# Performance work log

Measured on AMD Instinct MI355X. Metric: run time of the kernel, lower is better.

The kernel has to match this reference:

```python
import jax, jax.numpy as jnp
import numpy as np

EPS = 1e-5
D, C, T, H = 512, 256, 2, 2  # d_model, d_ctx, tokens, heads
HD = D // H                   # head dim


def _ln(x, g, b):
    m = x.mean(-1, keepdims=True)
    v = ((x - m) ** 2).mean(-1, keepdims=True)
    return (x - m) / jnp.sqrt(v + EPS) * g + b


def setup_inputs() -> dict:
    key = jax.random.key(0)
    ks = jax.random.split(key, 16)
    B, L = 8, 4096
    w = lambda k, s: (jax.random.normal(k, s, jnp.float32) * 0.02)
    Hc, H2 = 512, 1024  # ctx-head hidden = max(D,C); mix hidden = 2*D
    return {
        "x": jax.random.normal(ks[0], (B, L, D), jnp.float32),
        "context": jax.random.normal(ks[1], (B, C), jnp.float32),
        "pad_valid_mask": jax.random.bernoulli(ks[2], 0.9, (B, L)),
        "film_ln_g": jnp.ones(D), "film_ln_b": jnp.zeros(D),
        "film_w": w(ks[3], (2 * D, C)), "film_b": jnp.zeros(2 * D),
        "concat_w": w(ks[4], (D, D + C)), "concat_b": jnp.zeros(D),
        "concat_ln_g": jnp.ones(D), "concat_ln_b": jnp.zeros(D),
        "ctx_w1": w(ks[5], (Hc, C)), "ctx_b1": jnp.zeros(Hc),
        "ctx_w2": w(ks[6], (T * D, Hc)), "ctx_b2": jnp.zeros(T * D),
        "q_ln_g": jnp.ones(D), "q_ln_b": jnp.zeros(D),
        "in_proj_w": w(ks[7], (3 * D, D)), "in_proj_b": jnp.zeros(3 * D),
        "out_proj_w": w(ks[8], (D, D)), "out_proj_b": jnp.zeros(D),
        "mix_w1": w(ks[9], (H2, 4 * D)), "mix_b1": jnp.zeros(H2),
        "mix_w2": w(ks[10], (D, H2)), "mix_b2": jnp.zeros(D),
        "out_ln_g": jnp.ones(D), "out_ln_b": jnp.zeros(D),
        "gate_w": w(ks[11], (D, C)), "gate_b": jnp.zeros(D),
    }


def reference(x, context, pad_valid_mask,
              film_ln_g, film_ln_b, film_w, film_b,
              concat_w, concat_b, concat_ln_g, concat_ln_b,
              ctx_w1, ctx_b1, ctx_w2, ctx_b2,
              q_ln_g, q_ln_b, in_proj_w, in_proj_b, out_proj_w, out_proj_b,
              mix_w1, mix_b1, mix_w2, mix_b2,
              out_ln_g, out_ln_b, gate_w, gate_b):
    B, L, _ = x.shape
    film_gain, alpha_max = 1.0, 1.0
    # 1) HyperFiLM: base = (1 + gain*gamma) * LN(x) + gain*beta
    gb = context @ film_w.T + film_b                      # [B, 2D]
    gamma, beta = gb[:, :D], gb[:, D:]
    base = (1.0 + film_gain * gamma)[:, None, :] * _ln(x, film_ln_g, film_ln_b) \
           + (film_gain * beta)[:, None, :]
    # 2) Concat path
    ctx_exp = jnp.broadcast_to(context[:, None, :], (B, L, C))
    z = jnp.concatenate([x, ctx_exp], axis=-1)            # [B, L, D+C]
    upd_c = _ln(jax.nn.relu(z @ concat_w.T + concat_b), concat_ln_g, concat_ln_b)
    # 3) Cross-attn path: context -> T tokens
    h = jax.nn.gelu(context @ ctx_w1.T + ctx_b1, approximate=False)
    ctx_tok = (h @ ctx_w2.T + ctx_b2).reshape(B, T, D)
    x_q = _ln(x, q_ln_g, q_ln_b)
    wq, wk, wv = in_proj_w[:D], in_proj_w[D:2 * D], in_proj_w[2 * D:]
    bq, bk, bv = in_proj_b[:D], in_proj_b[D:2 * D], in_proj_b[2 * D:]
    q = (x_q @ wq.T + bq).reshape(B, L, H, HD)
    k = (ctx_tok @ wk.T + bk).reshape(B, T, H, HD)
    v = (ctx_tok @ wv.T + bv).reshape(B, T, H, HD)
    scores = jnp.einsum('blhd,bthd->bhlt', q, k) / jnp.sqrt(jnp.float32(HD))
    attn = jax.nn.softmax(scores, axis=-1)
    a = jnp.einsum('bhlt,bthd->blhd', attn, v).reshape(B, L, D)
    attn_out = a @ out_proj_w.T + out_proj_b
    mix_in = jnp.concatenate([x, attn_out, x - attn_out, x * attn_out], axis=-1)
    upd_a = jax.nn.relu(mix_in @ mix_w1.T + mix_b1) @ mix_w2.T + mix_b2
    # 4) Combine with sigmoid gate, alpha, pad mask
    gate = jax.nn.sigmoid(context @ gate_w.T + gate_b) * alpha_max  # [B, D]
    gate = gate[:, None, :] * pad_valid_mask[:, :, None].astype(x.dtype)
    out = _ln(base + gate * (upd_c + upd_a), out_ln_g, out_ln_b)
    return out
```

## Files before the change

### kernel.cpp

```cpp
#include <hip/hip_runtime.h>
#include <hip/hip_bf16.h>


#define N_TOK 32768
#define HALF_ROWS 16384

typedef unsigned short u16;
typedef __attribute__((ext_vector_type(8))) __bf16 bf16x8;
typedef __attribute__((ext_vector_type(4))) float f32x4;

__device__ __forceinline__ float bf2f(unsigned int h) { return __uint_as_float(h << 16); }
__device__ __forceinline__ u16 f2bf(float f) {
    unsigned int u = __float_as_uint(f);
    u += 0x7FFFu + ((u >> 16) & 1u);
    return (u16)(u >> 16);
}
__device__ __forceinline__ void load8(const u16* p, float* v) {
    uint4 u = *(const uint4*)p;
    v[0] = bf2f(u.x & 0xffffu); v[1] = bf2f(u.x >> 16);
    v[2] = bf2f(u.y & 0xffffu); v[3] = bf2f(u.y >> 16);
    v[4] = bf2f(u.z & 0xffffu); v[5] = bf2f(u.z >> 16);
    v[6] = bf2f(u.w & 0xffffu); v[7] = bf2f(u.w >> 16);
}
__device__ __forceinline__ uint4 pack8(const float* v) {
    uint4 u;
    u.x = (unsigned)f2bf(v[0]) | ((unsigned)f2bf(v[1]) << 16);
    u.y = (unsigned)f2bf(v[2]) | ((unsigned)f2bf(v[3]) << 16);
    u.z = (unsigned)f2bf(v[4]) | ((unsigned)f2bf(v[5]) << 16);
    u.w = (unsigned)f2bf(v[6]) | ((unsigned)f2bf(v[7]) << 16);
    return u;
}
__device__ __forceinline__ void async16(const u16* g, u16* lds) {
    __builtin_amdgcn_global_load_lds(
        (const __attribute__((address_space(1))) unsigned int*)g,
        (__attribute__((address_space(3))) unsigned int*)lds, 16, 0, 0);
}

#define FENCE() asm volatile("" ::: "memory")
#define BARRIER() do { FENCE(); __builtin_amdgcn_s_barrier(); FENCE(); } while (0)
#define WAITV(n) asm volatile("s_waitcnt vmcnt(" #n ")" ::: "memory")
#define LGKM0()  asm volatile("s_waitcnt lgkmcnt(0)" ::: "memory")

__device__ void foldq_body(unsigned bid, int tid,
                           const float* __restrict__ in_proj_w,
                           const float* __restrict__ in_proj_b,
                           const float* __restrict__ qb,
                           float* __restrict__ bqp) {
    const int wave = tid >> 6, lane = tid & 63;
    const int j = bid * 4 + wave;
    const int i = lane * 8;
    float4 w0 = *(const float4*)(in_proj_w + (size_t)j * 512 + i);
    float4 w1 = *(const float4*)(in_proj_w + (size_t)j * 512 + i + 4);
    float4 b0 = *(const float4*)(qb + i);
    float4 b1 = *(const float4*)(qb + i + 4);
    float p1 = w0.x*b0.x + w0.y*b0.y + w0.z*b0.z + w0.w*b0.w
             + w1.x*b1.x + w1.y*b1.y + w1.z*b1.z + w1.w*b1.w;
    for (int m = 1; m < 64; m <<= 1) p1 += __shfl_xor(p1, m, 64);
    if (lane == 0) bqp[j] = in_proj_b[j] + p1;
}

__device__ void ctx_a_body(unsigned task, int tid,
                           const float* __restrict__ context,
                           const float* __restrict__ film_w, const float* __restrict__ film_b,
                           const float* __restrict__ gate_w, const float* __restrict__ gate_b,
                           const float* __restrict__ ctx_w1, const float* __restrict__ ctx_b1,
                           float* __restrict__ gb1, float* __restrict__ betab,
                           float* __restrict__ gateb, float* __restrict__ hbuf) {
    const int wave = tid >> 6, lane = tid & 63;
    const int widx = (int)task * 4 + wave;
    const int b   = widx >> 11;
    const int j2  = widx & 2047;
    const int cat = j2 >> 9;
    const int j   = j2 & 511;
    const float* wrow;
    if      (cat == 0) wrow = film_w + (size_t)j * 256;
    else if (cat == 1) wrow = film_w + (size_t)(512 + j) * 256;
    else if (cat == 2) wrow = gate_w + (size_t)j * 256;
    else               wrow = ctx_w1 + (size_t)j * 256;
    float4 wv = *(const float4*)(wrow + lane * 4);
    float4 cv = *(const float4*)(context + b * 256 + lane * 4);
    float s = wv.x * cv.x + wv.y * cv.y + wv.z * cv.z + wv.w * cv.w;
    for (int m = 1; m < 64; m <<= 1) s += __shfl_xor(s, m, 64);
    if (lane == 0) {
        if      (cat == 0) gb1[b * 512 + j]   = 1.0f + s + film_b[j];
        else if (cat == 1) betab[b * 512 + j] = s + film_b[512 + j];
        else if (cat == 2) gateb[b * 512 + j] = 1.f / (1.f + expf(-(s + gate_b[j])));
        else {
            float hv = s + ctx_b1[j];
            hbuf[b * 512 + j] = 0.5f * hv * (1.0f + erff(hv * 0.70710678118654752f));
        }
    }
}

__global__ void prep_ctxa_kernel(const float* __restrict__ in_proj_w,
                                 const float* __restrict__ in_proj_b,
                                 const float* __restrict__ qb,
                                 const float* __restrict__ context,
                                 float* __restrict__ bqp, u16* __restrict__ ctxbf,
                                 float* __restrict__ subuf,
                                 const float* __restrict__ film_w, const float* __restrict__ film_b,
                                 const float* __restrict__ gate_w, const float* __restrict__ gate_b,
                                 const float* __restrict__ ctx_w1, const float* __restrict__ ctx_b1,
                                 float* __restrict__ gb1, float* __restrict__ betab,
                                 float* __restrict__ gateb, float* __restrict__ hbuf) {
    const int tid = threadIdx.x;
    if (blockIdx.x < 128) {
        foldq_body(blockIdx.x, tid, in_proj_w, in_proj_b, qb, bqp);
    } else if (blockIdx.x == 128) {
        for (int i = tid; i < 2048; i += 256)
            ctxbf[i] = f2bf(context[i]);
        if (tid < 32) subuf[tid] = 0.f;
    } else {
        ctx_a_body(blockIdx.x - 129, tid, context, film_w, film_b,
                   gate_w, gate_b, ctx_w1, ctx_b1, gb1, betab, gateb, hbuf);
    }
}

__global__ void ctx_stage_b(const float* __restrict__ hbuf,
                            const float* __restrict__ ctx_w2, const float* __restrict__ ctx_b2,
                            float* __restrict__ tokbuf) {
    const int wave = threadIdx.x >> 6, lane = threadIdx.x & 63;
    const int widx = blockIdx.x * 4 + wave;
    const int b = widx >> 10;
    const int j = widx & 1023;
    const float* wrow = ctx_w2 + (size_t)j * 512 + lane * 8;
    const float* hr   = hbuf + b * 512 + lane * 8;
    float4 w0 = *(const float4*)wrow, w1 = *(const float4*)(wrow + 4);
    float4 h0 = *(const float4*)hr,   h1 = *(const float4*)(hr + 4);
    float s = w0.x*h0.x + w0.y*h0.y + w0.z*h0.z + w0.w*h0.w
            + w1.x*h1.x + w1.y*h1.y + w1.z*h1.z + w1.w*h1.w;
    for (int m = 1; m < 64; m <<= 1) s += __shfl_xor(s, m, 64);
    if (lane == 0) tokbuf[b * 1024 + j] = s + ctx_b2[j];
}

__global__ void ctx_stage_c(const float* __restrict__ tokbuf,
                            const float* __restrict__ in_proj_w, const float* __restrict__ in_proj_b,
                            float* __restrict__ kbuf, float* __restrict__ vbuf) {
    const int wave = threadIdx.x >> 6, lane = threadIdx.x & 63;
    const int widx = blockIdx.x * 4 + wave;
    const int b  = widx >> 11;
    const int r  = widx & 2047;
    const int t  = r >> 10;
    const int kv = (r >> 9) & 1;
    const int j  = r & 511;
    const float* wrow = in_proj_w + (size_t)(512 + kv * 512 + j) * 512 + lane * 8;
    const float* tk   = tokbuf + (b * 2 + t) * 512 + lane * 8;
    float4 w0 = *(const float4*)wrow, w1 = *(const float4*)(wrow + 4);
    float4 t0 = *(const float4*)tk,   t1 = *(const float4*)(tk + 4);
    float s = w0.x*t0.x + w0.y*t0.y + w0.z*t0.z + w0.w*t0.w
            + w1.x*t1.x + w1.y*t1.y + w1.z*t1.z + w1.w*t1.w;
    for (int m = 1; m < 64; m <<= 1) s += __shfl_xor(s, m, 64);
    if (lane == 0) {
        float v = s + in_proj_b[512 + kv * 512 + j];
        if (kv == 0) kbuf[(b * 2 + t) * 512 + j] = v;
        else         vbuf[(b * 2 + t) * 512 + j] = v;
    }
}

__global__ void ctx_stage_d2(const float* __restrict__ in_proj_w,
                             const float* __restrict__ out_proj_w,
                             const float* __restrict__ qg, const float* __restrict__ bqp,
                             const float* __restrict__ kbuf, const float* __restrict__ vbuf,
                             float* __restrict__ ubuf, float* __restrict__ vobuf,
                             float* __restrict__ subuf, float* __restrict__ c0buf) {
    const int tid = threadIdx.x;
    __shared__ float sh[256];
    __shared__ float red[256];
    if (blockIdx.x < 64) {
        const int task = blockIdx.x >> 1, jh = blockIdx.x & 1;
        const int b = task >> 2, idx = task & 3;
        const int t = idx >> 1, h = idx & 1;
        const int j = jh * 256 + tid;
        sh[tid] = kbuf[(b * 2 + t) * 512 + h * 256 + tid];
        __syncthreads();
        float a = 0.f;
        #pragma unroll 4
        for (int dd = 0; dd < 256; dd++)
            a += sh[dd] * in_proj_w[(size_t)(h * 256 + dd) * 512 + j];
        float u = a * qg[j];
        ubuf[task * 512 + j] = u;
        red[tid] = u;
        __syncthreads();
        for (int s = 128; s > 0; s >>= 1) { if (tid < s) red[tid] += red[tid + s]; __syncthreads(); }
        if (tid == 0) atomicAdd(&subuf[task], red[0]);
        if (jh == 0) {
            __syncthreads();
            red[tid] = bqp[h * 256 + tid] * sh[tid];
            __syncthreads();
            for (int s = 128; s > 0; s >>= 1) { if (tid < s) red[tid] += red[tid + s]; __syncthreads(); }
            if (tid == 0) c0buf[task] = red[0];
        }
    } else {
        const int r = blockIdx.x - 64;
        const int task = r >> 1, jh = r & 1;
        const int b = task >> 2, idx = task & 3;
        const int t = idx >> 1, h = idx & 1;
        const int j = jh * 256 + tid;
        sh[tid] = vbuf[(b * 2 + t) * 512 + h * 256 + tid];
        __syncthreads();
        const float* w0 = out_proj_w + (size_t)j * 512 + h * 256;
        float acc0 = 0.f;
        #pragma unroll 2
        for (int dd = 0; dd < 256; dd += 4) {
            float4 x0 = *(const float4*)(w0 + dd);
            acc0 += x0.x*sh[dd] + x0.y*sh[dd+1] + x0.z*sh[dd+2] + x0.w*sh[dd+3];
        }
        vobuf[task * 512 + j] = acc0;
    }
}

__device__ void statsattn_body(unsigned task, int tid, int rowbase,
                               const float* __restrict__ x, float* __restrict__ stats,
                               u16* __restrict__ mixA, u16* __restrict__ pbufH,
                               const float* __restrict__ ubuf, const float* __restrict__ subuf,
                               const float* __restrict__ c0buf, const float* __restrict__ vobuf,
                               const float* __restrict__ ob) {
    const int wave = tid >> 6, lane = tid & 63;
    const size_t lr = (size_t)task * 8 + wave * 2;
    const size_t gr = lr + rowbase;
    const int b = (int)(gr >> 12);
    float v[2][8], s[2] = {0.f, 0.f}, ss[2] = {0.f, 0.f};
    #pragma unroll
    for (int r = 0; r < 2; r++) {
        const float* xr = x + (gr + r) * 512 + lane * 8;
        float4 a = *(const float4*)xr;
        float4 c = *(const float4*)(xr + 4);
        v[r][0]=a.x; v[r][1]=a.y; v[r][2]=a.z; v[r][3]=a.w;
        v[r][4]=c.x; v[r][5]=c.y; v[r][6]=c.z; v[r][7]=c.w;
        #pragma unroll
        for (int e = 0; e < 8; e++) { s[r] += v[r][e]; ss[r] += v[r][e] * v[r][e]; }
    }
    float u[4][8];
    #pragma unroll
    for (int idx = 0; idx < 4; idx++) {
        const float* up = ubuf + (b * 4 + idx) * 512 + lane * 8;
        float4 u0 = *(const float4*)up, u1 = *(const float4*)(up + 4);
        u[idx][0]=u0.x; u[idx][1]=u0.y; u[idx][2]=u0.z; u[idx][3]=u0.w;
        u[idx][4]=u1.x; u[idx][5]=u1.y; u[idx][6]=u1.z; u[idx][7]=u1.w;
    }
    float sd[2][4];
    #pragma unroll
    for (int r = 0; r < 2; r++)
        #pragma unroll
        for (int idx = 0; idx < 4; idx++) {
            float acc = 0.f;
            #pragma unroll
            for (int e = 0; e < 8; e++) acc += v[r][e] * u[idx][e];
            sd[r][idx] = acc;
        }
    for (int m = 1; m < 64; m <<= 1) {
        #pragma unroll
        for (int r = 0; r < 2; r++) {
            s[r] += __shfl_xor(s[r], m, 64); ss[r] += __shfl_xor(ss[r], m, 64);
            #pragma unroll
            for (int idx = 0; idx < 4; idx++) sd[r][idx] += __shfl_xor(sd[r][idx], m, 64);
        }
    }
    float vo[4][8];
    #pragma unroll
    for (int idx = 0; idx < 4; idx++) {
        const float* vp = vobuf + (b * 4 + idx) * 512 + lane * 8;
        float4 v0 = *(const float4*)vp, v1 = *(const float4*)(vp + 4);
        vo[idx][0]=v0.x; vo[idx][1]=v0.y; vo[idx][2]=v0.z; vo[idx][3]=v0.w;
        vo[idx][4]=v1.x; vo[idx][5]=v1.y; vo[idx][6]=v1.z; vo[idx][7]=v1.w;
    }
    float obp[8];
    {
        const float* op = ob + lane * 8;
        float4 o0 = *(const float4*)op, o1 = *(const float4*)(op + 4);
        obp[0]=o0.x; obp[1]=o0.y; obp[2]=o0.z; obp[3]=o0.w;
        obp[4]=o1.x; obp[5]=o1.y; obp[6]=o1.z; obp[7]=o1.w;
    }
    #pragma unroll
    for (int r = 0; r < 2; r++) {
        const float mean = s[r] * (1.f / 512.f);
        const float rstd = rsqrtf(ss[r] * (1.f / 512.f) - mean * mean + 1e-5f);
        if (lane == 0) { stats[(gr + r) * 2] = mean; stats[(gr + r) * 2 + 1] = rstd; }
        float sc[4];
        #pragma unroll
        for (int idx = 0; idx < 4; idx++)
            sc[idx] = (rstd * (sd[r][idx] - mean * subuf[b * 4 + idx]) + c0buf[b * 4 + idx]) * (1.f / 16.f);
        float p[4];
        #pragma unroll
        for (int h = 0; h < 2; h++) {
            float s0 = sc[h], s1 = sc[2 + h];
            float mx = fmaxf(s0, s1);
            float e0 = expf(s0 - mx), e1 = expf(s1 - mx);
            float inv = 1.f / (e0 + e1);
            p[h] = e0 * inv; p[2 + h] = e1 * inv;
        }
        float o[8], pr[8];
        #pragma unroll
        for (int e = 0; e < 8; e++) {
            o[e] = p[0]*vo[0][e] + p[1]*vo[1][e] + p[2]*vo[2][e] + p[3]*vo[3][e] + obp[e];
            pr[e] = v[r][e] * o[e];
        }
        *(uint4*)(mixA + (gr + r) * 1024 + lane * 8)       = pack8(v[r]);
        *(uint4*)(mixA + (gr + r) * 1024 + 512 + lane * 8) = pack8(o);
        *(uint4*)(pbufH + (lr + r) * 512 + lane * 8)       = pack8(pr);
    }
}

__device__ void wconv_body(unsigned t, int tid,
                           const float* __restrict__ concat_w,
                           const float* __restrict__ mix_w1,
                           const float* __restrict__ mix_w2,
                           u16* __restrict__ cwbf, u16* __restrict__ m1bf,
                           u16* __restrict__ m2bf) {
    if (t < 192) {
        int i = t * 256 + tid;
        const float* s = concat_w + (size_t)i * 8;
        float4 a = *(const float4*)s;
        float4 b = *(const float4*)(s + 4);
        float v[8] = {a.x, a.y, a.z, a.w, b.x, b.y, b.z, b.w};
        *(uint4*)(cwbf + (size_t)i * 8) = pack8(v);
    } else if (t < 448) {
        int i = (t - 192) * 256 + tid;
        const float* s = mix_w2 + (size_t)i * 8;
        float4 a = *(const float4*)s;
        float4 b = *(const float4*)(s + 4);
        float v[8] = {a.x, a.y, a.z, a.w, b.x, b.y, b.z, b.w};
        *(uint4*)(m2bf + (size_t)i * 8) = pack8(v);
    } else {
        int idx = (t - 448) * 256 + tid;
        int n = idx / 192;
        int k = (idx - n * 192) * 8;
        const float* base = mix_w1 + (size_t)n * 2048;
        float v[8];
        if (k < 512) {
            #pragma unroll
            for (int e = 0; e < 8; e++) v[e] = base[k + e] + base[1024 + k + e];
        } else if (k < 1024) {
            #pragma unroll
            for (int e = 0; e < 8; e++) v[e] = base[k + e] - base[512 + k + e];
        } else {
            #pragma unroll
            for (int e = 0; e < 8; e++) v[e] = base[512 + k + e];
        }
        *(uint4*)(m1bf + (size_t)n * 1536 + k) = pack8(v);
    }
}

__global__ void statsattn_kernel(const float* __restrict__ x, float* __restrict__ stats,
                                 u16* __restrict__ mixA, u16* __restrict__ pbufH,
                                 const float* __restrict__ ubuf, const float* __restrict__ subuf,
                                 const float* __restrict__ c0buf, const float* __restrict__ vobuf,
                                 const float* __restrict__ ob, const int rowbase,
                                 const int ntasks,
                                 const float* __restrict__ concat_w,
                                 const float* __restrict__ mix_w1,
                                 const float* __restrict__ mix_w2,
                                 u16* __restrict__ cwbf, u16* __restrict__ m1bf,
                                 u16* __restrict__ m2bf) {
    if ((int)blockIdx.x < ntasks)
        statsattn_body(blockIdx.x, threadIdx.x, rowbase, x, stats, mixA, pbufH,
                       ubuf, subuf, c0buf, vobuf, ob);
    else
        wconv_body(blockIdx.x - ntasks, threadIdx.x, concat_w, mix_w1, mix_w2,
                   cwbf, m1bf, m2bf);
}

template<int AMODE, int NT, bool RELU>
__device__ __forceinline__ void gemm8_body(const u16* __restrict__ A0, const u16* __restrict__ A1,
                                           const u16* __restrict__ Wb, const float* __restrict__ bias,
                                           u16* __restrict__ out, const int ldo,
                                           const int bx, const int by, u16* S) {
    constexpr int BLD = NT * 64;
    constexpr int NIT = NT / 2;
    u16* As = S;
    u16* Bs = S + 32768;
    const int tid = threadIdx.x;
    const int l = tid & 63;
    const int w = tid >> 6;
    const int wm = w >> 2, wn = w & 3;
    const int quad = l >> 4, lc = l & 15;
    const size_t m0 = (size_t)bx * 256;
    const int n0 = by * 256;
    const int bidx = (int)(m0 >> 12);

    const int r0 = tid >> 3;
    const int r1 = (tid + 512) >> 3;
    const int c0s = ((tid & 7) ^ (r0 & 7)) * 8;
    const int c1s = ((tid & 7) ^ (r1 & 7)) * 8;

    auto stA = [&](int kt, int h, int buf) {
        u16* dst = As + (buf * 2 + h) * 8192;
        if constexpr (AMODE == 0) {
            async16(A0 + (m0 + h * 128 + r0) * 1024 + kt * 64 + c0s, dst + tid * 8);
            async16(A0 + (m0 + h * 128 + r1) * 1024 + kt * 64 + c1s, dst + (tid + 512) * 8);
        } else if constexpr (AMODE == 1) {
            if (kt < 8) {
                async16(A0 + (m0 + h * 128 + r0) * 1024 + kt * 64 + c0s, dst + tid * 8);
                async16(A0 + (m0 + h * 128 + r1) * 1024 + kt * 64 + c1s, dst + (tid + 512) * 8);
            } else {
                async16(A1 + bidx * 256 + (kt - 8) * 64 + c0s, dst + tid * 8);
                async16(A1 + bidx * 256 + (kt - 8) * 64 + c1s, dst + (tid + 512) * 8);
            }
        } else {
            if (kt < 16) {
                async16(A0 + (m0 + h * 128 + r0) * 1024 + kt * 64 + c0s, dst + tid * 8);
                async16(A0 + (m0 + h * 128 + r1) * 1024 + kt * 64 + c1s, dst + (tid + 512) * 8);
            } else {
                async16(A1 + (m0 + h * 128 + r0) * 512 + (kt - 16) * 64 + c0s, dst + tid * 8);
                async16(A1 + (m0 + h * 128 + r1) * 512 + (kt - 16) * 64 + c1s, dst + (tid + 512) * 8);
            }
        }
    };
    auto stB = [&](int kt, int h, int buf) {
        u16* dst = Bs + (buf * 2 + h) * 8192;
        async16(Wb + (size_t)(n0 + h * 128 + r0) * BLD + kt * 64 + c0s, dst + tid * 8);
        async16(Wb + (size_t)(n0 + h * 128 + r1) * BLD + kt * 64 + c1s, dst + (tid + 512) * 8);
    };

    bf16x8 a_[4][2], b_[2][2][2];
    f32x4 acc[8][4];
    #pragma unroll
    for (int i = 0; i < 8; i++)
        #pragma unroll
        for (int j = 0; j < 4; j++) acc[i][j] = (f32x4){0.f, 0.f, 0.f, 0.f};

    auto rdA = [&](int buf, int qi) {
        const u16* Ab = As + (buf * 2 + wm) * 8192;
        #pragma unroll
        for (int ii = 0; ii < 4; ii++) {
            const int r = (qi * 4 + ii) * 16 + lc;
            #pragma unroll
            for (int kk = 0; kk < 2; kk++) {
                const int cs = (kk * 4 + quad) ^ (r & 7);
                a_[ii][kk] = *(const bf16x8*)&Ab[r * 64 + cs * 8];
            }
        }
    };
    auto rdB = [&](int buf, int qj) {
        #pragma unroll
        for (int jj = 0; jj < 2; jj++) {
            const int nr = wn * 64 + (qj * 2 + jj) * 16 + lc;
            const int hb = nr >> 7, r = nr & 127;
            const u16* Bb = Bs + (buf * 2 + hb) * 8192;
            #pragma unroll
            for (int kk = 0; kk < 2; kk++) {
                const int cs = (kk * 4 + quad) ^ (r & 7);
                b_[qj][jj][kk] = *(const bf16x8*)&Bb[r * 64 + cs * 8];
            }
        }
    };
    auto mfma16 = [&](int qi, int qj) {
        __builtin_amdgcn_s_setprio(1);
        #pragma unroll
        for (int ii = 0; ii < 4; ii++)
            #pragma unroll
            for (int jj = 0; jj < 2; jj++)
                #pragma unroll
                for (int kk = 0; kk < 2; kk++)
                    acc[qi * 4 + ii][qj * 2 + jj] = __builtin_amdgcn_mfma_f32_16x16x32_bf16(
                        a_[ii][kk], b_[qj][jj][kk], acc[qi * 4 + ii][qj * 2 + jj], 0, 0, 0);
        __builtin_amdgcn_s_setprio(0);
    };

    stA(0, 0, 0); stA(0, 1, 0); stB(0, 0, 0); stB(0, 1, 0);
    stA(1, 0, 1);
    WAITV(2); BARRIER();

    for (int it = 0; it < NIT; it++) {
        const int tb = 2 * it + 1;
        const bool more = (it < NIT - 1);
        rdA(0, 0); rdB(0, 0);
        stA(tb, 1, 1);
        BARRIER(); mfma16(0, 0);
        rdB(0, 1);
        stB(tb, 0, 1);
        BARRIER(); mfma16(0, 1);
        rdA(0, 1);
        stB(tb, 1, 1);
        BARRIER(); mfma16(1, 1);
        BARRIER();
        if (more) { stA(tb + 1, 0, 0); WAITV(2); }
        else      { WAITV(0); }
        BARRIER(); mfma16(1, 0);
        rdA(1, 0); rdB(1, 0);
        if (more) stA(tb + 1, 1, 0);
        BARRIER(); mfma16(0, 0);
        rdB(1, 1);
        if (more) stB(tb + 1, 0, 0);
        BARRIER(); mfma16(0, 1);
        rdA(1, 1);
        if (more) stB(tb + 1, 1, 0);
        BARRIER(); mfma16(1, 1);
        BARRIER();
        if (more) { stA(tb + 2, 0, 1); WAITV(2); }
        BARRIER(); mfma16(1, 0);
    }

    BARRIER();
    float bv[4];
    #pragma unroll
    for (int j = 0; j < 4; j++) bv[j] = bias[n0 + wn * 64 + j * 16 + lc];
    #pragma unroll
    for (int p = 0; p < 2; p++) {
        if (p) BARRIER();
        if (wm == p) {
            #pragma unroll
            for (int i = 0; i < 8; i++)
                #pragma unroll
                for (int j = 0; j < 4; j++)
                    #pragma unroll
                    for (int reg = 0; reg < 4; reg++) {
                        float vv = acc[i][j][reg] + bv[j];
                        if (RELU) vv = fmaxf(vv, 0.f);
                        S[(i * 16 + quad * 4 + reg) * 264 + wn * 64 + j * 16 + lc] = f2bf(vv);
                    }
        }
        LGKM0(); BARRIER();
        #pragma unroll
        for (int kq = 0; kq < 8; kq++) {
            const int cix = tid + kq * 512;
            const int row = cix >> 5, ch = cix & 31;
            *(uint4*)(out + (m0 + p * 128 + row) * (size_t)ldo + n0 + ch * 8)
                = *(const uint4*)&S[row * 264 + ch * 8];
        }
    }
}

template<int AMODE, int NT, bool RELU>
__launch_bounds__(512, 2)
__global__ void mix_gemm8(const u16* __restrict__ A0, const u16* __restrict__ A1,
                          const u16* __restrict__ Wb, const float* __restrict__ bias,
                          u16* __restrict__ out, const int ldo) {
    extern __shared__ __align__(16) u16 S[];
    gemm8_body<AMODE, NT, RELU>(A0, A1, Wb, bias, out, ldo, blockIdx.x, blockIdx.y, S);
}

__launch_bounds__(512, 2)
__global__ void mix2_concat_kernel(const u16* __restrict__ bufh, const u16* __restrict__ m2bf,
                                   const float* __restrict__ mix_b2, u16* __restrict__ out_a,
                                   const u16* __restrict__ mixA, const u16* __restrict__ ctxbf,
                                   const u16* __restrict__ cwbf, const float* __restrict__ concat_b,
                                   u16* __restrict__ bufc) {
    extern __shared__ __align__(16) u16 S[];
    if (blockIdx.x < 128)
        gemm8_body<0, 16, false>(bufh, nullptr, m2bf, mix_b2, out_a, 1024,
                                 blockIdx.x, blockIdx.y, S);
    else
        gemm8_body<1, 12, true>(mixA, ctxbf, cwbf, concat_b, bufc, 512,
                                blockIdx.x - 128, blockIdx.y, S);
}

__global__ void final_kernel(const u16* __restrict__ mixA, const float* __restrict__ stats,
                             const u16* __restrict__ bufc,
                             const float* __restrict__ cg_, const float* __restrict__ cb,
                             const float* __restrict__ gb1, const float* __restrict__ betab,
                             const float* __restrict__ gateb, const int* __restrict__ mask,
                             const float* __restrict__ fg, const float* __restrict__ fb,
                             const float* __restrict__ og, const float* __restrict__ ob,
                             float* __restrict__ out) {
    const int wave = threadIdx.x >> 6, lane = threadIdx.x & 63;
    const size_t row = (size_t)blockIdx.x * 4 + wave;
    const int b = (int)(row >> 12);
    const int c0 = lane * 8;
    float xv[8], uc[8], ua[8];
    load8(mixA + row * 1024 + c0, xv);
    load8(mixA + row * 1024 + 512 + c0, ua);
    load8(bufc + row * 512 + c0, uc);
    float sc = 0.f, ssc = 0.f;
    #pragma unroll
    for (int e = 0; e < 8; e++) { sc += uc[e]; ssc += uc[e] * uc[e]; }
    for (int m = 1; m < 64; m <<= 1) { sc += __shfl_xor(sc, m, 64); ssc += __shfl_xor(ssc, m, 64); }
    const float mc = sc * (1.f / 512.f);
    const float rc = rsqrtf(ssc * (1.f / 512.f) - mc * mc + 1e-5f);
    const float mean = stats[row * 2], rstd = stats[row * 2 + 1];
    const float mf = (mask[row] != 0) ? 1.f : 0.f;
    float y[8];
    float s = 0.f, ss = 0.f;
    #pragma unroll
    for (int e = 0; e < 8; e++) {
        int c = c0 + e;
        float ucn = (uc[e] - mc) * rc * cg_[c] + cb[c];
        float xh = (xv[e] - mean) * rstd;
        float base = gb1[b * 512 + c] * (xh * fg[c] + fb[c]) + betab[b * 512 + c];
        float yv = base + gateb[b * 512 + c] * mf * (ucn + ua[e]);
        y[e] = yv; s += yv; ss += yv * yv;
    }
    for (int m = 1; m < 64; m <<= 1) { s += __shfl_xor(s, m, 64); ss += __shfl_xor(ss, m, 64); }
    float mean2 = s * (1.f / 512.f);
    float rstd2 = rsqrtf(ss * (1.f / 512.f) - mean2 * mean2 + 1e-5f);
    float o[8];
    #pragma unroll
    for (int e = 0; e < 8; e++) {
        int c = c0 + e;
        o[e] = (y[e] - mean2) * rstd2 * og[c] + ob[c];
    }
    *(float4*)(out + row * 512 + c0)     = make_float4(o[0], o[1], o[2], o[3]);
    *(float4*)(out + row * 512 + c0 + 4) = make_float4(o[4], o[5], o[6], o[7]);
}

extern "C" void kernel_launch(void* const* d_in, const int* in_sizes, int n_in,
                              void* d_out, int out_size, void* d_ws, size_t ws_size,
                              hipStream_t stream) {
    const float* x          = (const float*)d_in[0];
    const float* context    = (const float*)d_in[1];
    const int*   mask       = (const int*)d_in[2];
    const float* film_ln_g  = (const float*)d_in[3];
    const float* film_ln_b  = (const float*)d_in[4];
    const float* film_w     = (const float*)d_in[5];
    const float* film_b     = (const float*)d_in[6];
    const float* concat_w   = (const float*)d_in[7];
    const float* concat_b   = (const float*)d_in[8];
    const float* concat_ln_g= (const float*)d_in[9];
    const float* concat_ln_b= (const float*)d_in[10];
    const float* ctx_w1     = (const float*)d_in[11];
    const float* ctx_b1     = (const float*)d_in[12];
    const float* ctx_w2     = (const float*)d_in[13];
    const float* ctx_b2     = (const float*)d_in[14];
    const float* q_ln_g     = (const float*)d_in[15];
    const float* q_ln_b     = (const float*)d_in[16];
    const float* in_proj_w  = (const float*)d_in[17];
    const float* in_proj_b  = (const float*)d_in[18];
    const float* out_proj_w = (const float*)d_in[19];
    const float* out_proj_b = (const float*)d_in[20];
    const float* mix_w1     = (const float*)d_in[21];
    const float* mix_b1     = (const float*)d_in[22];
    const float* mix_w2     = (const float*)d_in[23];
    const float* mix_b2     = (const float*)d_in[24];
    const float* out_ln_g   = (const float*)d_in[25];
    const float* out_ln_b   = (const float*)d_in[26];
    const float* gate_w     = (const float*)d_in[27];
    const float* gate_b     = (const float*)d_in[28];
    float* out = (float*)d_out;

    float* gb1    = (float*)d_ws;
    float* betab  = gb1 + 4096;
    float* gateb  = betab + 4096;
    float* kbuf   = gateb + 4096;
    float* vbuf   = kbuf + 8192;
    float* bqp    = vbuf + 8192;
    float* hbuf   = bqp + 512;
    float* tokbuf = hbuf + 4096;
    float* ubuf   = tokbuf + 8192;
    float* vobuf  = ubuf + 16384;
    float* subuf  = vobuf + 16384;
    float* c0buf  = subuf + 32;
    float* stats  = c0buf + 32;
    u16* ctxbf = (u16*)(stats + 65536);
    u16* cwbf  = ctxbf + 2048;
    u16* m1bf  = cwbf + 393216;
    u16* m2bf  = m1bf + 1572864;
    u16* mixA  = m2bf + 524288;
    u16* bufh  = mixA + (size_t)N_TOK * 1024;
    u16* pbuf  = bufh + (size_t)N_TOK * 1024;

    const bool full = (ws_size >= 173316352ull);

    static bool attr_set = false;
    if (!attr_set) {
        hipFuncSetAttribute(reinterpret_cast<const void*>(&mix_gemm8<2, 24, true>),
                            hipFuncAttributeMaxDynamicSharedMemorySize, 131072);
        hipFuncSetAttribute(reinterpret_cast<const void*>(&mix_gemm8<0, 16, false>),
                            hipFuncAttributeMaxDynamicSharedMemorySize, 131072);
        hipFuncSetAttribute(reinterpret_cast<const void*>(&mix_gemm8<1, 12, true>),
                            hipFuncAttributeMaxDynamicSharedMemorySize, 131072);
        hipFuncSetAttribute(reinterpret_cast<const void*>(&mix2_concat_kernel),
                            hipFuncAttributeMaxDynamicSharedMemorySize, 131072);
        attr_set = true;
    }

    prep_ctxa_kernel<<<4225, 256, 0, stream>>>(
        in_proj_w, in_proj_b, q_ln_b, context,
        bqp, ctxbf, subuf,
        film_w, film_b, gate_w, gate_b, ctx_w1, ctx_b1,
        gb1, betab, gateb, hbuf);
    ctx_stage_b<<<2048, 256, 0, stream>>>(hbuf, ctx_w2, ctx_b2, tokbuf);
    ctx_stage_c<<<4096, 256, 0, stream>>>(tokbuf, in_proj_w, in_proj_b, kbuf, vbuf);
    ctx_stage_d2<<<128, 256, 0, stream>>>(in_proj_w, out_proj_w, q_ln_g, bqp,
                                          kbuf, vbuf, ubuf, vobuf, subuf, c0buf);

    if (full) {
        u16* bufc = pbuf;
        statsattn_kernel<<<4096 + 1216, 256, 0, stream>>>(
            x, stats, mixA, pbuf, ubuf, subuf, c0buf, vobuf, out_proj_b,
            0, 4096, concat_w, mix_w1, mix_w2, cwbf, m1bf, m2bf);
        mix_gemm8<2, 24, true><<<dim3(128, 4), 512, 131072, stream>>>(
            mixA, pbuf, m1bf, mix_b1, bufh, 1024);
        mix2_concat_kernel<<<dim3(256, 2), 512, 131072, stream>>>(
            bufh, m2bf, mix_b2, mixA + 512,
            mixA, ctxbf, cwbf, concat_b, bufc);
        final_kernel<<<N_TOK / 4, 256, 0, stream>>>(mixA, stats, bufc,
                                                    concat_ln_g, concat_ln_b,
                                                    gb1, betab, gateb, mask,
                                                    film_ln_g, film_ln_b,
                                                    out_ln_g, out_ln_b, out);
    } else {
        u16* bufc = bufh;
        for (int h = 0; h < 2; h++) {
            const int rowbase = h * HALF_ROWS;
            const int nconv = (h == 0) ? 1216 : 0;
            statsattn_kernel<<<2048 + nconv, 256, 0, stream>>>(
                x, stats, mixA, pbuf, ubuf, subuf, c0buf, vobuf, out_proj_b,
                rowbase, 2048, concat_w, mix_w1, mix_w2, cwbf, m1bf, m2bf);
            mix_gemm8<2, 24, true><<<dim3(64, 4), 512, 131072, stream>>>(
                mixA + (size_t)rowbase * 1024, pbuf, m1bf, mix_b1,
                bufh + (size_t)rowbase * 1024, 1024);
        }
        mix_gemm8<0, 16, false><<<dim3(128, 2), 512, 131072, stream>>>(
            bufh, nullptr, m2bf, mix_b2, mixA + 512, 1024);
        mix_gemm8<1, 12, true><<<dim3(128, 2), 512, 131072, stream>>>(
            mixA, ctxbf, cwbf, concat_b, bufc, 512);
        final_kernel<<<N_TOK / 4, 256, 0, stream>>>(mixA, stats, bufc,
                                                    concat_ln_g, concat_ln_b,
                                                    gb1, betab, gateb, mask,
                                                    film_ln_g, film_ln_b,
                                                    out_ln_g, out_ln_b, out);
    }
    (void)in_sizes; (void)n_in; (void)out_size; (void)ws_size;
}
```

Baseline: 418.1 us.

## Move x layernorm stats and weight conversion into the small context-chain kernels

The per-row LN statistics and bf16 copy of x, plus the weight bf16 conversion, are split out of the attention kernel and folded as extra blocks into the latency-bound ctx_stage_b and ctx_stage_c launches. This fills otherwise idle GPU capacity during the serial context chain. The later attention kernel now rereads x as bf16 from mixA and reads stats from memory. That halves its x read traffic but adds a stats read, and it computes attention scores from bf16-rounded x rather than fp32.

```diff
diff --git a/kernel.cpp b/kernel.cpp
--- a/kernel.cpp
+++ b/kernel.cpp
@@ -116,11 +116,83 @@
     }
 }
 
-__global__ void ctx_stage_b(const float* __restrict__ hbuf,
-                            const float* __restrict__ ctx_w2, const float* __restrict__ ctx_b2,
-                            float* __restrict__ tokbuf) {
-    const int wave = threadIdx.x >> 6, lane = threadIdx.x & 63;
-    const int widx = blockIdx.x * 4 + wave;
+__device__ void xstats_body(unsigned task, int tid,
+                            const float* __restrict__ x, float* __restrict__ stats,
+                            u16* __restrict__ mixA) {
+    const int wave = tid >> 6, lane = tid & 63;
+    const size_t gr = (size_t)task * 8 + wave * 2;
+    float v[2][8], s[2] = {0.f, 0.f}, ss[2] = {0.f, 0.f};
+    #pragma unroll
+    for (int r = 0; r < 2; r++) {
+        const float* xr = x + (gr + r) * 512 + lane * 8;
+        float4 a = *(const float4*)xr;
+        float4 c = *(const float4*)(xr + 4);
+        v[r][0]=a.x; v[r][1]=a.y; v[r][2]=a.z; v[r][3]=a.w;
+        v[r][4]=c.x; v[r][5]=c.y; v[r][6]=c.z; v[r][7]=c.w;
+        #pragma unroll
+        for (int e = 0; e < 8; e++) { s[r] += v[r][e]; ss[r] += v[r][e] * v[r][e]; }
+    }
+    for (int m = 1; m < 64; m <<= 1) {
+        #pragma unroll
+        for (int r = 0; r < 2; r++) {
+            s[r] += __shfl_xor(s[r], m, 64); ss[r] += __shfl_xor(ss[r], m, 64);
+        }
+    }
+    #pragma unroll
+    for (int r = 0; r < 2; r++) {
+        const float mean = s[r] * (1.f / 512.f);
+        const float rstd = rsqrtf(ss[r] * (1.f / 512.f) - mean * mean + 1e-5f);
+        if (lane == 0) { stats[(gr + r) * 2] = mean; stats[(gr + r) * 2 + 1] = rstd; }
+        *(uint4*)(mixA + (gr + r) * 1024 + lane * 8) = pack8(v[r]);
+    }
+}
+
+__device__ void wconv_body(unsigned t, int tid,
+                           const float* __restrict__ concat_w,
+                           const float* __restrict__ mix_w1,
+                           const float* __restrict__ mix_w2,
+                           u16* __restrict__ cwbf, u16* __restrict__ m1bf,
+                           u16* __restrict__ m2bf) {
+    if (t < 192) {
+        int i = t * 256 + tid;
+        const float* s = concat_w + (size_t)i * 8;
+        float4 a = *(const float4*)s;
+        float4 b = *(const float4*)(s + 4);
+        float v[8] = {a.x, a.y, a.z, a.w, b.x, b.y, b.z, b.w};
+        *(uint4*)(cwbf + (size_t)i * 8) = pack8(v);
+    } else if (t < 448) {
+        int i = (t - 192) * 256 + tid;
+        const float* s = mix_w2 + (size_t)i * 8;
+        float4 a = *(const float4*)s;
+        float4 b = *(const float4*)(s + 4);
+        float v[8] = {a.x, a.y, a.z, a.w, b.x, b.y, b.z, b.w};
+        *(uint4*)(m2bf + (size_t)i * 8) = pack8(v);
+    } else {
+        int idx = (t - 448) * 256 + tid;
+        int n = idx / 192;
+        int k = (idx - n * 192) * 8;
+        const float* base = mix_w1 + (size_t)n * 2048;
+        float v[8];
+        if (k < 512) {
+            #pragma unroll
+            for (int e = 0; e < 8; e++) v[e] = base[k + e] + base[1024 + k + e];
+        } else if (k < 1024) {
+            #pragma unroll
+            for (int e = 0; e < 8; e++) v[e] = base[k + e] - base[512 + k + e];
+        } else {
+            #pragma unroll
+            for (int e = 0; e < 8; e++) v[e] = base[512 + k + e];
+        }
+        *(uint4*)(m1bf + (size_t)n * 1536 + k) = pack8(v);
+    }
+}
+
+__device__ void ctx_b_body(unsigned task, int tid,
+                           const float* __restrict__ hbuf,
+                           const float* __restrict__ ctx_w2, const float* __restrict__ ctx_b2,
+                           float* __restrict__ tokbuf) {
+    const int wave = tid >> 6, lane = tid & 63;
+    const int widx = (int)task * 4 + wave;
     const int b = widx >> 10;
     const int j = widx & 1023;
     const float* wrow = ctx_w2 + (size_t)j * 512 + lane * 8;
@@ -133,11 +205,31 @@
     if (lane == 0) tokbuf[b * 1024 + j] = s + ctx_b2[j];
 }
 
-__global__ void ctx_stage_c(const float* __restrict__ tokbuf,
-                            const float* __restrict__ in_proj_w, const float* __restrict__ in_proj_b,
-                            float* __restrict__ kbuf, float* __restrict__ vbuf) {
-    const int wave = threadIdx.x >> 6, lane = threadIdx.x & 63;
-    const int widx = blockIdx.x * 4 + wave;
+__global__ void ctx_b_kernel(const float* __restrict__ hbuf,
+                             const float* __restrict__ ctx_w2, const float* __restrict__ ctx_b2,
+                             float* __restrict__ tokbuf,
+                             const float* __restrict__ x, float* __restrict__ stats,
+                             u16* __restrict__ mixA,
+                             const float* __restrict__ concat_w,
+                             const float* __restrict__ mix_w1,
+                             const float* __restrict__ mix_w2,
+                             u16* __restrict__ cwbf, u16* __restrict__ m1bf,
+                             u16* __restrict__ m2bf) {
+    if (blockIdx.x < 2048)
+        ctx_b_body(blockIdx.x, threadIdx.x, hbuf, ctx_w2, ctx_b2, tokbuf);
+    else if (blockIdx.x < 4096)
+        xstats_body(blockIdx.x - 2048, threadIdx.x, x, stats, mixA);
+    else
+        wconv_body(blockIdx.x - 4096, threadIdx.x, concat_w, mix_w1, mix_w2,
+                   cwbf, m1bf, m2bf);
+}
+
+__device__ void ctx_c_body(unsigned task, int tid,
+                           const float* __restrict__ tokbuf,
+                           const float* __restrict__ in_proj_w, const float* __restrict__ in_proj_b,
+                           float* __restrict__ kbuf, float* __restrict__ vbuf) {
+    const int wave = tid >> 6, lane = tid & 63;
+    const int widx = (int)task * 4 + wave;
     const int b  = widx >> 11;
     const int r  = widx & 2047;
     const int t  = r >> 10;
@@ -155,6 +247,17 @@
         if (kv == 0) kbuf[(b * 2 + t) * 512 + j] = v;
         else         vbuf[(b * 2 + t) * 512 + j] = v;
     }
+}
+
+__global__ void ctx_c_kernel(const float* __restrict__ tokbuf,
+                             const float* __restrict__ in_proj_w, const float* __restrict__ in_proj_b,
+                             float* __restrict__ kbuf, float* __restrict__ vbuf,
+                             const float* __restrict__ x, float* __restrict__ stats,
+                             u16* __restrict__ mixA) {
+    if (blockIdx.x < 4096)
+        ctx_c_body(blockIdx.x, threadIdx.x, tokbuf, in_proj_w, in_proj_b, kbuf, vbuf);
+    else
+        xstats_body(2048 + blockIdx.x - 4096, threadIdx.x, x, stats, mixA);
 }
 
 __global__ void ctx_stage_d2(const float* __restrict__ in_proj_w,
@@ -209,27 +312,19 @@
     }
 }
 
-__device__ void statsattn_body(unsigned task, int tid, int rowbase,
-                               const float* __restrict__ x, float* __restrict__ stats,
-                               u16* __restrict__ mixA, u16* __restrict__ pbufH,
-                               const float* __restrict__ ubuf, const float* __restrict__ subuf,
-                               const float* __restrict__ c0buf, const float* __restrict__ vobuf,
-                               const float* __restrict__ ob) {
-    const int wave = tid >> 6, lane = tid & 63;
-    const size_t lr = (size_t)task * 8 + wave * 2;
+__global__ void attn2_kernel(float* __restrict__ stats,
+                             u16* __restrict__ mixA, u16* __restrict__ pbufH,
+                             const float* __restrict__ ubuf, const float* __restrict__ subuf,
+                             const float* __restrict__ c0buf, const float* __restrict__ vobuf,
+                             const float* __restrict__ ob, const int rowbase) {
+    const int wave = threadIdx.x >> 6, lane = threadIdx.x & 63;
+    const size_t lr = (size_t)blockIdx.x * 8 + wave * 2;
     const size_t gr = lr + rowbase;
     const int b = (int)(gr >> 12);
-    float v[2][8], s[2] = {0.f, 0.f}, ss[2] = {0.f, 0.f};
-    #pragma unroll
-    for (int r = 0; r < 2; r++) {
-        const float* xr = x + (gr + r) * 512 + lane * 8;
-        float4 a = *(const float4*)xr;
-        float4 c = *(const float4*)(xr + 4);
-        v[r][0]=a.x; v[r][1]=a.y; v[r][2]=a.z; v[r][3]=a.w;
-        v[r][4]=c.x; v[r][5]=c.y; v[r][6]=c.z; v[r][7]=c.w;
-        #pragma unroll
-        for (int e = 0; e < 8; e++) { s[r] += v[r][e]; ss[r] += v[r][e] * v[r][e]; }
-    }
+    float v[2][8];
+    #pragma unroll
+    for (int r = 0; r < 2; r++)
+        load8(mixA + (gr + r) * 1024 + lane * 8, v[r]);
     float u[4][8];
     #pragma unroll
     for (int idx = 0; idx < 4; idx++) {
@@ -250,11 +345,9 @@
         }
     for (int m = 1; m < 64; m <<= 1) {
         #pragma unroll
-        for (int r = 0; r < 2; r++) {
-            s[r] += __shfl_xor(s[r], m, 64); ss[r] += __shfl_xor(ss[r], m, 64);
+        for (int r = 0; r < 2; r++)
             #pragma unroll
             for (int idx = 0; idx < 4; idx++) sd[r][idx] += __shfl_xor(sd[r][idx], m, 64);
-        }
     }
     float vo[4][8];
     #pragma unroll
@@ -273,9 +366,8 @@
     }
     #pragma unroll
     for (int r = 0; r < 2; r++) {
-        const float mean = s[r] * (1.f / 512.f);
-        const float rstd = rsqrtf(ss[r] * (1.f / 512.f) - mean * mean + 1e-5f);
-        if (lane == 0) { stats[(gr + r) * 2] = mean; stats[(gr + r) * 2 + 1] = rstd; }
+        const float mean = stats[(gr + r) * 2];
+        const float rstd = stats[(gr + r) * 2 + 1];
         float sc[4];
         #pragma unroll
         for (int idx = 0; idx < 4; idx++)
@@ -295,69 +387,9 @@
             o[e] = p[0]*vo[0][e] + p[1]*vo[1][e] + p[2]*vo[2][e] + p[3]*vo[3][e] + obp[e];
             pr[e] = v[r][e] * o[e];
         }
-        *(uint4*)(mixA + (gr + r) * 1024 + lane * 8)       = pack8(v[r]);
         *(uint4*)(mixA + (gr + r) * 1024 + 512 + lane * 8) = pack8(o);
         *(uint4*)(pbufH + (lr + r) * 512 + lane * 8)       = pack8(pr);
     }
-}
-
-__device__ void wconv_body(unsigned t, int tid,
-                           const float* __restrict__ concat_w,
-                           const float* __restrict__ mix_w1,
-                           const float* __restrict__ mix_w2,
-                           u16* __restrict__ cwbf, u16* __restrict__ m1bf,
-                           u16* __restrict__ m2bf) {
-    if (t < 192) {
-        int i = t * 256 + tid;
-        const float* s = concat_w + (size_t)i * 8;
-        float4 a = *(const float4*)s;
-        float4 b = *(const float4*)(s + 4);
-        float v[8] = {a.x, a.y, a.z, a.w, b.x, b.y, b.z, b.w};
-        *(uint4*)(cwbf + (size_t)i * 8) = pack8(v);
-    } else if (t < 448) {
-        int i = (t - 192) * 256 + tid;
-        const float* s = mix_w2 + (size_t)i * 8;
-        float4 a = *(const float4*)s;
-        float4 b = *(const float4*)(s + 4);
-        float v[8] = {a.x, a.y, a.z, a.w, b.x, b.y, b.z, b.w};
-        *(uint4*)(m2bf + (size_t)i * 8) = pack8(v);
-    } else {
-        int idx = (t - 448) * 256 + tid;
-        int n = idx / 192;
-        int k = (idx - n * 192) * 8;
-        const float* base = mix_w1 + (size_t)n * 2048;
-        float v[8];
-        if (k < 512) {
-            #pragma unroll
-            for (int e = 0; e < 8; e++) v[e] = base[k + e] + base[1024 + k + e];
-        } else if (k < 1024) {
-            #pragma unroll
-            for (int e = 0; e < 8; e++) v[e] = base[k + e] - base[512 + k + e];
-        } else {
-            #pragma unroll
-            for (int e = 0; e < 8; e++) v[e] = base[512 + k + e];
-        }
-        *(uint4*)(m1bf + (size_t)n * 1536 + k) = pack8(v);
-    }
-}
-
-__global__ void statsattn_kernel(const float* __restrict__ x, float* __restrict__ stats,
-                                 u16* __restrict__ mixA, u16* __restrict__ pbufH,
-                                 const float* __restrict__ ubuf, const float* __restrict__ subuf,
-                                 const float* __restrict__ c0buf, const float* __restrict__ vobuf,
-                                 const float* __restrict__ ob, const int rowbase,
-                                 const int ntasks,
-                                 const float* __restrict__ concat_w,
-                                 const float* __restrict__ mix_w1,
-                                 const float* __restrict__ mix_w2,
-                                 u16* __restrict__ cwbf, u16* __restrict__ m1bf,
-                                 u16* __restrict__ m2bf) {
-    if ((int)blockIdx.x < ntasks)
-        statsattn_body(blockIdx.x, threadIdx.x, rowbase, x, stats, mixA, pbufH,
-                       ubuf, subuf, c0buf, vobuf, ob);
-    else
-        wconv_body(blockIdx.x - ntasks, threadIdx.x, concat_w, mix_w1, mix_w2,
-                   cwbf, m1bf, m2bf);
 }
 
 template<int AMODE, int NT, bool RELU>
@@ -668,16 +700,19 @@
         bqp, ctxbf, subuf,
         film_w, film_b, gate_w, gate_b, ctx_w1, ctx_b1,
         gb1, betab, gateb, hbuf);
-    ctx_stage_b<<<2048, 256, 0, stream>>>(hbuf, ctx_w2, ctx_b2, tokbuf);
-    ctx_stage_c<<<4096, 256, 0, stream>>>(tokbuf, in_proj_w, in_proj_b, kbuf, vbuf);
+    ctx_b_kernel<<<5312, 256, 0, stream>>>(hbuf, ctx_w2, ctx_b2, tokbuf,
+                                           x, stats, mixA,
+                                           concat_w, mix_w1, mix_w2,
+                                           cwbf, m1bf, m2bf);
+    ctx_c_kernel<<<6144, 256, 0, stream>>>(tokbuf, in_proj_w, in_proj_b, kbuf, vbuf,
+                                           x, stats, mixA);
     ctx_stage_d2<<<128, 256, 0, stream>>>(in_proj_w, out_proj_w, q_ln_g, bqp,
                                           kbuf, vbuf, ubuf, vobuf, subuf, c0buf);
 
     if (full) {
         u16* bufc = pbuf;
-        statsattn_kernel<<<4096 + 1216, 256, 0, stream>>>(
-            x, stats, mixA, pbuf, ubuf, subuf, c0buf, vobuf, out_proj_b,
-            0, 4096, concat_w, mix_w1, mix_w2, cwbf, m1bf, m2bf);
+        attn2_kernel<<<N_TOK / 8, 256, 0, stream>>>(
+            stats, mixA, pbuf, ubuf, subuf, c0buf, vobuf, out_proj_b, 0);
         mix_gemm8<2, 24, true><<<dim3(128, 4), 512, 131072, stream>>>(
             mixA, pbuf, m1bf, mix_b1, bufh, 1024);
         mix2_concat_kernel<<<dim3(256, 2), 512, 131072, stream>>>(
@@ -692,10 +727,8 @@
         u16* bufc = bufh;
         for (int h = 0; h < 2; h++) {
             const int rowbase = h * HALF_ROWS;
-            const int nconv = (h == 0) ? 1216 : 0;
-            statsattn_kernel<<<2048 + nconv, 256, 0, stream>>>(
-                x, stats, mixA, pbuf, ubuf, subuf, c0buf, vobuf, out_proj_b,
-                rowbase, 2048, concat_w, mix_w1, mix_w2, cwbf, m1bf, m2bf);
+            attn2_kernel<<<HALF_ROWS / 8, 256, 0, stream>>>(
+                stats, mixA, pbuf, ubuf, subuf, c0buf, vobuf, out_proj_b, rowbase);
             mix_gemm8<2, 24, true><<<dim3(64, 4), 512, 131072, stream>>>(
                 mixA + (size_t)rowbase * 1024, pbuf, m1bf, mix_b1,
                 bufh + (size_t)rowbase * 1024, 1024);
```

Result: no change. 426.3 us (+2.0%).
